# Kernel optimization log

Hardware: AMD Instinct MI355X
Metric: run time of the kernel (lower is better)

The kernel has to match this reference:

```python
import jax, jax.numpy as jnp
import numpy as np

DIM = 2048
NUM_HEADS = 16
NUM_KV_HEADS = 4
HEAD_DIM = DIM // NUM_HEADS
KV_DIM = NUM_KV_HEADS * HEAD_DIM
ROPE_BASE = 10000.0
QK_GAIN_INIT = 1.0
BSZ, SEQ = 4, 2048


def rms_norm(x):
    eps = jnp.finfo(x.dtype).eps
    return x * jax.lax.rsqrt(jnp.mean(x * x, axis=-1, keepdims=True) + eps)


def rope_cos_sin(seqlen, head_dim, base, dtype):
    inv_freq = base ** (-jnp.arange(0, head_dim, 2, dtype=jnp.float32) / head_dim)
    t = jnp.arange(seqlen, dtype=jnp.float32)
    freqs = t[:, None] * inv_freq[None, :]  # [S, hd/2]
    return jnp.cos(freqs).astype(dtype), jnp.sin(freqs).astype(dtype)


def apply_rotary(x, cos, sin):
    # x: [B, H, S, hd]; cos/sin: [S, hd/2]
    x1, x2 = jnp.split(x, 2, axis=-1)
    c = cos[None, None, :, :]
    s = sin[None, None, :, :]
    return jnp.concatenate([x1 * c + x2 * s, -x1 * s + x2 * c], axis=-1)


def setup_inputs() -> dict:
    key = jax.random.key(0)
    ks = jax.random.split(key, 6)
    std = 0.02
    return {
        "x": jax.random.normal(ks[0], (BSZ, SEQ, DIM), dtype=jnp.float32),
        "Wq": jax.random.normal(ks[1], (DIM, DIM), dtype=jnp.float32) * std,
        "Wk": jax.random.normal(ks[2], (KV_DIM, DIM), dtype=jnp.float32) * std,
        "Wv": jax.random.normal(ks[3], (KV_DIM, DIM), dtype=jnp.float32) * std,
        "Wo": jax.random.normal(ks[4], (DIM, DIM), dtype=jnp.float32) * std,
        "q_gain": jnp.full((NUM_HEADS,), QK_GAIN_INIT, dtype=jnp.float32),
    }


def reference(x, Wq, Wk, Wv, Wo, q_gain):
    bsz, seqlen, dim = x.shape
    # QKV projections (F.linear: x @ W.T)
    q = (x @ Wq.T).reshape(bsz, seqlen, NUM_HEADS, HEAD_DIM).transpose(0, 2, 1, 3)
    k = (x @ Wk.T).reshape(bsz, seqlen, NUM_KV_HEADS, HEAD_DIM).transpose(0, 2, 1, 3)
    v = (x @ Wv.T).reshape(bsz, seqlen, NUM_KV_HEADS, HEAD_DIM).transpose(0, 2, 1, 3)
    # QK RMSNorm
    q = rms_norm(q)
    k = rms_norm(k)
    # RoPE
    cos, sin = rope_cos_sin(seqlen, HEAD_DIM, ROPE_BASE, q.dtype)
    q = apply_rotary(q, cos, sin)
    k = apply_rotary(k, cos, sin)
    # per-head gain
    q = q * q_gain.astype(q.dtype)[None, :, None, None]
    # GQA: repeat kv heads
    rep = NUM_HEADS // NUM_KV_HEADS
    k = jnp.repeat(k, rep, axis=1)
    v = jnp.repeat(v, rep, axis=1)
    # causal SDPA
    scale = 1.0 / jnp.sqrt(jnp.asarray(HEAD_DIM, dtype=q.dtype))
    scores = jnp.einsum("bhsd,bhtd->bhst", q, k) * scale
    causal = jnp.tril(jnp.ones((seqlen, seqlen), dtype=bool))
    scores = jnp.where(causal[None, None], scores, jnp.asarray(-jnp.inf, scores.dtype))
    attn = jax.nn.softmax(scores, axis=-1)
    y = jnp.einsum("bhst,bhtd->bhsd", attn, v)
    y = y.transpose(0, 2, 1, 3).reshape(bsz, seqlen, dim)
    return y @ Wo.T
```

## Files before the change

kernel.cpp:

```cpp
#include <hip/hip_runtime.h>
#include <hip/hip_bf16.h>

typedef __hip_bfloat16 bf16;
typedef short s16x8 __attribute__((ext_vector_type(8)));
typedef float f32x4 __attribute__((ext_vector_type(4)));

#define DIM 2048
#define NHEADS 16
#define NKVH 4
#define HD 128
#define KVDIM 512
#define BSZ 4
#define SEQ 2048
#define MROWS (BSZ*SEQ)
#define NQKV (DIM+2*KVDIM)

__device__ __forceinline__ void gld_lds16(const bf16* g, short* l) {
  __builtin_amdgcn_global_load_lds((__attribute__((address_space(1))) void*)(void*)g,
                                   (__attribute__((address_space(3))) void*)l, 16, 0, 0);
}

__global__ __launch_bounds__(256) void cast_bf16(const float* __restrict__ src,
                                                 bf16* __restrict__ dst, int n8) {
  int i = blockIdx.x*256 + threadIdx.x;
  if (i >= n8) return;
  const float4* s4 = (const float4*)src;
  float4 a = s4[2*i];
  float4 b = s4[2*i+1];
  union { bf16 h[8]; uint4 u; } o;
  o.h[0] = __float2bfloat16(a.x); o.h[1] = __float2bfloat16(a.y);
  o.h[2] = __float2bfloat16(a.z); o.h[3] = __float2bfloat16(a.w);
  o.h[4] = __float2bfloat16(b.x); o.h[5] = __float2bfloat16(b.y);
  o.h[6] = __float2bfloat16(b.z); o.h[7] = __float2bfloat16(b.w);
  ((uint4*)dst)[i] = o.u;
}

__global__ __launch_bounds__(256) void cast_w3(const float* __restrict__ Wq,
                                               const float* __restrict__ Wk,
                                               const float* __restrict__ Wv,
                                               bf16* __restrict__ dst) {
  int i = blockIdx.x*256 + threadIdx.x;
  const float* src; int j;
  if (i < 524288)      { src = Wq; j = i; }
  else if (i < 655360) { src = Wk; j = i - 524288; }
  else                 { src = Wv; j = i - 655360; }
  const float4* s4 = (const float4*)src;
  float4 a = s4[2*j];
  float4 b = s4[2*j+1];
  union { bf16 h[8]; uint4 u; } o;
  o.h[0] = __float2bfloat16(a.x); o.h[1] = __float2bfloat16(a.y);
  o.h[2] = __float2bfloat16(a.z); o.h[3] = __float2bfloat16(a.w);
  o.h[4] = __float2bfloat16(b.x); o.h[5] = __float2bfloat16(b.y);
  o.h[6] = __float2bfloat16(b.z); o.h[7] = __float2bfloat16(b.w);
  ((uint4*)dst)[i] = o.u;
}


template<int MQ>
__device__ __forceinline__ void lda(s16x8 (&af)[4][2], const short* pa, int rds) {
#pragma unroll
  for (int fr = 0; fr < 4; fr++)
#pragma unroll
    for (int ks = 0; ks < 2; ks++)
      af[fr][ks] = *(const s16x8*)(pa + ((MQ*4 + fr)*2 + ks)*512 + rds);
}
template<int NQ>
__device__ __forceinline__ void ldb(s16x8 (&bfv)[2][2], const short* pb, int bsub, int rds) {
#pragma unroll
  for (int fc = 0; fc < 2; fc++)
#pragma unroll
    for (int ks = 0; ks < 2; ks++)
      bfv[fc][ks] = *(const s16x8*)(pb + (bsub + (NQ*2 + fc)*2 + ks)*512 + rds);
}
template<int MQ, int NQ>
__device__ __forceinline__ void mmq(f32x4 (&acc)[8][4], const s16x8 (&af)[4][2],
                                    const s16x8 (&bfv)[2][2]) {
#pragma unroll
  for (int fr = 0; fr < 4; fr++)
#pragma unroll
    for (int fc = 0; fc < 2; fc++)
#pragma unroll
      for (int ks = 0; ks < 2; ks++)
        acc[MQ*4+fr][NQ*2+fc] = __builtin_amdgcn_mfma_f32_16x16x32_bf16(
            af[fr][ks], bfv[fc][ks], acc[MQ*4+fr][NQ*2+fc], 0, 0, 0);
}

#define WV6 asm volatile("s_waitcnt vmcnt(6)" ::: "memory")
#define WV0 asm volatile("s_waitcnt vmcnt(0)" ::: "memory")
#define WVN ((void)0)
#define GBAR __builtin_amdgcn_s_barrier()
#define WLK asm volatile("s_waitcnt lgkmcnt(0)" ::: "memory")
#define PRI1 __builtin_amdgcn_s_setprio(1)
#define PRI0 __builtin_amdgcn_s_setprio(0)

#define KT(B_, T_, S1_, S2_, WVX) do {                                          \
    const short* pa = pAr[B_];                                                  \
    const short* pb = pBr[B_];                                                  \
    s16x8 af[4][2], b0f[2][2], b1f[2][2];                                       \
                                                        \
    lda<0>(af, pa, rds); ldb<0>(b0f, pb, bsub, rds);                            \
    if (S1_) {                                                                  \
      gld_lds16(Ab +      (long)((T_)+1)*64 + eA1, &L[1-(B_)][0][4096+wid512]); \
      gld_lds16(Ab + h1 + (long)((T_)+1)*64 + eA1, &L[1-(B_)][1][4096+wid512]); \
    }                                                                           \
    GBAR; WLK; PRI1; mmq<0,0>(acc, af, b0f); PRI0; GBAR;                        \
                                                        \
    ldb<1>(b1f, pb, bsub, rds);                                                 \
    if (S2_) {                                                                  \
      gld_lds16(Ab +      (long)((T_)+2)*64 + eA0, &L[B_][0][wid512]);          \
      gld_lds16(Ab + h1 + (long)((T_)+2)*64 + eA0, &L[B_][1][wid512]);          \
    }                                                                           \
    GBAR; WLK; PRI1; mmq<0,1>(acc, af, b1f); PRI0; GBAR;                        \
                                                        \
    lda<1>(af, pa, rds);                                                        \
    if (S2_) {                                                                  \
      gld_lds16(Bb + (long)((T_)+2)*64 + eA0, &L[B_][2][wid512]);               \
      gld_lds16(Bb + (long)((T_)+2)*64 + eA1, &L[B_][2][4096+wid512]);          \
    }                                                                           \
    GBAR; WLK; PRI1; mmq<1,0>(acc, af, b0f); PRI0; GBAR;                        \
                                                        \
    if (S2_) {                                                                  \
      gld_lds16(Bb + h1 + (long)((T_)+2)*64 + eA0, &L[B_][3][wid512]);          \
      gld_lds16(Bb + h1 + (long)((T_)+2)*64 + eA1, &L[B_][3][4096+wid512]);     \
    }                                                                           \
    WVX;                                                                        \
    GBAR; PRI1; mmq<1,1>(acc, af, b1f); PRI0; GBAR;                             \
  } while (0)

template<int EPI>
__global__ __launch_bounds__(512, 2) void gemm8(
    const bf16* __restrict__ A, const bf16* __restrict__ Bm,
    float* __restrict__ Cf, bf16* __restrict__ Qo, bf16* __restrict__ Ko,
    bf16* __restrict__ Vo, int N, int K) {
  __shared__ short L[2][4][8192] __attribute__((aligned(16)));
  const int tid = threadIdx.x;
  const int lane = tid & 63, wid = tid >> 6;
  const int quad = lane >> 4, l15 = lane & 15;
  const int wm = wid >> 2, wn = wid & 3;
  const int m0 = blockIdx.y * 256, n0 = blockIdx.x * 256;

  const int rds = l15*32 + ((quad*8) ^ ((l15 & 8) << 1));
  const int bsub = (wn & 1) * 8;

  const int colx = ((lane & 3) * 8) ^ ((lane >> 5) << 4);
  const int gc   = ((wid & 1) << 5) + colx;
  const int gr0  = ((wid >> 1) << 4) + (lane >> 2);
  const long eA0 = (long)gr0 * K + gc;
  const long eA1 = eA0 + 64L * K;
  const int wid512 = wid * 512;
  const bf16* Ab = A  + (long)m0 * K;
  const bf16* Bb = Bm + (long)n0 * K;
  const long h1 = 128L * K;

  const short* pAr[2] = { &L[0][wm][0], &L[1][wm][0] };
  const short* pBr[2] = { &L[0][2 + (wn >> 1)][0], &L[1][2 + (wn >> 1)][0] };

  f32x4 acc[8][4] = {};

  gld_lds16(Ab + eA0,           &L[0][0][wid512]);
  gld_lds16(Ab + eA1,           &L[0][0][4096 + wid512]);
  gld_lds16(Ab + h1 + eA0,      &L[0][1][wid512]);
  gld_lds16(Ab + h1 + eA1,      &L[0][1][4096 + wid512]);
  gld_lds16(Bb + eA0,           &L[0][2][wid512]);
  gld_lds16(Bb + eA1,           &L[0][2][4096 + wid512]);
  gld_lds16(Bb + h1 + eA0,      &L[0][3][wid512]);
  gld_lds16(Bb + h1 + eA1,      &L[0][3][4096 + wid512]);
  gld_lds16(Ab + 64 + eA0,      &L[1][0][wid512]);
  gld_lds16(Ab + h1 + 64 + eA0, &L[1][1][wid512]);
  gld_lds16(Bb + 64 + eA0,      &L[1][2][wid512]);
  gld_lds16(Bb + 64 + eA1,      &L[1][2][4096 + wid512]);
  gld_lds16(Bb + h1 + 64 + eA0, &L[1][3][wid512]);
  gld_lds16(Bb + h1 + 64 + eA1, &L[1][3][4096 + wid512]);
  WV6;
  GBAR;

  for (int t = 0; t < 30; t += 2) {
    KT(0, t,   1, 1, WV6);
    KT(1, t+1, 1, 1, WV6);
  }
  KT(0, 30, 1, 0, WV0);
  KT(1, 31, 0, 0, WVN);

#pragma unroll
  for (int mi = 0; mi < 8; mi++) {
#pragma unroll
    for (int nj = 0; nj < 4; nj++) {
      const int col = n0 + wn*64 + nj*16 + l15;
#pragma unroll
      for (int r = 0; r < 4; r++) {
        const int row = m0 + wm*128 + mi*16 + quad*4 + r;
        const float v = acc[mi][nj][r];
        if (EPI == 0) {
          Cf[(long)row*N + col] = v;
        } else {
          const int b = row >> 11, s = row & (SEQ-1);
          const bf16 hv = __float2bfloat16(v);
          if (col < DIM) {
            const int h = col >> 7, d = col & 127;
            Qo[((long)(b*NHEADS + h)*SEQ + s)*HD + d] = hv;
          } else if (col < DIM + KVDIM) {
            const int c2 = col - DIM, h = c2 >> 7, d = c2 & 127;
            Ko[((long)(b*NKVH + h)*SEQ + s)*HD + d] = hv;
          } else {
            const int c2 = col - DIM - KVDIM, h = c2 >> 7, d = c2 & 127;
            Vo[((long)(b*NKVH + h)*HD + d)*SEQ + s] = hv;
          }
        }
      }
    }
  }
}

__global__ __launch_bounds__(256) void norm_rope(bf16* __restrict__ Qb,
                                                 bf16* __restrict__ Kb,
                                                 const float* __restrict__ gain) {
  const int lane = threadIdx.x & 63, wid = threadIdx.x >> 6;
  const long rid = (long)blockIdx.x*4 + wid;
  const long QR = (long)BSZ*NHEADS*SEQ;
  bf16* ptr; float g; int s;
  if (rid < QR) {
    ptr = Qb + rid*HD;
    s = (int)(rid & (SEQ-1));
    const int h = (int)((rid >> 11) & 15);
    g = gain[h] * 0.08838834764831845f;
  } else {
    const long r2 = rid - QR;
    ptr = Kb + r2*HD;
    s = (int)(r2 & (SEQ-1));
    g = 1.0f;
  }
  float x1 = __bfloat162float(ptr[lane]);
  float x2 = __bfloat162float(ptr[lane+64]);
  float ss = x1*x1 + x2*x2;
#pragma unroll
  for (int off = 1; off < 64; off <<= 1) ss += __shfl_xor(ss, off);
  const float rn = rsqrtf(ss*(1.0f/128.0f) + 1.1920928955078125e-07f);
  const float inv_freq = exp2f((float)lane * -0.20762050593046014f);
  float sn, cs;
  sincosf((float)s * inv_freq, &sn, &cs);
  const float q1 = x1*rn, q2 = x2*rn;
  ptr[lane]    = __float2bfloat16((q1*cs + q2*sn)*g);
  ptr[lane+64] = __float2bfloat16((q2*cs - q1*sn)*g);
}

__global__ __launch_bounds__(256, 2) void attn(
    const bf16* __restrict__ Qb, const bf16* __restrict__ Kb,
    const bf16* __restrict__ Vtg, bf16* __restrict__ Yb) {
  __shared__ short Kt[64*136]  __attribute__((aligned(16)));
  __shared__ short Vt[128*72]  __attribute__((aligned(16)));
  __shared__ short Pt[4*2304]  __attribute__((aligned(16)));

  const int tid = threadIdx.x;
  const int lane = tid & 63, wid = tid >> 6;
  const int quad = lane >> 4, l15 = lane & 15;
  const int xb = blockIdx.x;
  const int bh = blockIdx.y;
  const int b = bh >> 4, h = bh & 15, kvh = h >> 2;

  const bf16* kbase = Kb  + (long)(b*NKVH + kvh)*SEQ*HD;
  const bf16* vbase = Vtg + (long)(b*NKVH + kvh)*HD*SEQ;
  short* pw0 = Pt + wid*2304;
  short* pw1 = pw0 + 1152;
  const int krow = tid >> 4, kc = (tid & 15)*8;
  const int vrow = tid >> 3, vc = (tid & 7)*8;

  for (int phase = 0; phase < 2; phase++) {
    const int qt = phase ? xb : (15 - xb);
    const int q0 = qt*128 + wid*16 + l15;
    const int q1 = q0 + 64;
    const bf16* qr0 = Qb + ((long)(b*NHEADS + h)*SEQ + q0)*HD + quad*8;
    s16x8 qa0[4], qa1[4];
#pragma unroll
    for (int st = 0; st < 4; st++) {
      qa0[st] = *(const s16x8*)(qr0 + st*32);
      qa1[st] = *(const s16x8*)(qr0 + 64*HD + st*32);
    }

    f32x4 o0[8] = {}, o1[8] = {};
    float li0 = 0.0f, li1 = 0.0f;
    const int ktiles = 2*qt + 2;

    for (int kt = 0; kt < ktiles; kt++) {
      __syncthreads();
#pragma unroll
      for (int i = 0; i < 4; i++) {
        uint4 kv = *(const uint4*)(kbase + (long)(kt*64 + i*16 + krow)*HD + kc);
        *(uint4*)&Kt[(i*16 + krow)*136 + kc] = kv;
      }
#pragma unroll
      for (int i = 0; i < 4; i++) {
        uint4 vv = *(const uint4*)(vbase + (long)(i*32 + vrow)*SEQ + kt*64 + vc);
        *(uint4*)&Vt[(i*32 + vrow)*72 + vc] = vv;
      }
      __syncthreads();

      f32x4 s0[4] = {}, s1[4] = {};
#pragma unroll
      for (int nt = 0; nt < 4; nt++) {
        s16x8 kf[4];
#pragma unroll
        for (int st = 0; st < 4; st++)
          kf[st] = *(const s16x8*)&Kt[(nt*16 + l15)*136 + st*32 + quad*8];
#pragma unroll
        for (int st = 0; st < 4; st++) {
          s0[nt] = __builtin_amdgcn_mfma_f32_16x16x32_bf16(kf[st], qa0[st], s0[nt], 0, 0, 0);
          s1[nt] = __builtin_amdgcn_mfma_f32_16x16x32_bf16(kf[st], qa1[st], s1[nt], 0, 0, 0);
        }
      }

      const bool d0 = (kt >= 2*qt);
      const bool d1 = (kt >  2*qt);
      const int tb = kt*64 + quad*4;
      union { bf16 h[16]; unsigned long long u[4]; } p0, p1;
      float rs0 = 0.0f, rs1 = 0.0f;
#pragma unroll
      for (int nt = 0; nt < 4; nt++) {
#pragma unroll
        for (int r = 0; r < 4; r++) {
          const int t = tb + nt*16 + r;
          float v0 = s0[nt][r], v1 = s1[nt][r];
          if (d0 && (t > q0)) v0 = -1e30f;
          if (d1 && (t > q1)) v1 = -1e30f;
          const float e0 = __expf(v0 - 12.0f);
          const float e1 = __expf(v1 - 12.0f);
          rs0 += e0; rs1 += e1;
          p0.h[nt*4+r] = __float2bfloat16(e0);
          p1.h[nt*4+r] = __float2bfloat16(e1);
        }
      }
      li0 += rs0; li1 += rs1;
#pragma unroll
      for (int nt = 0; nt < 4; nt++) {
        *(unsigned long long*)&pw0[l15*72 + nt*16 + quad*4] = p0.u[nt];
        *(unsigned long long*)&pw1[l15*72 + nt*16 + quad*4] = p1.u[nt];
      }

#pragma unroll
      for (int st = 0; st < 2; st++) {
        s16x8 pf0 = *(const s16x8*)&pw0[l15*72 + st*32 + quad*8];
        s16x8 pf1 = *(const s16x8*)&pw1[l15*72 + st*32 + quad*8];
#pragma unroll
        for (int dt = 0; dt < 8; dt++) {
          s16x8 vf = *(const s16x8*)&Vt[(dt*16 + l15)*72 + st*32 + quad*8];
          o0[dt] = __builtin_amdgcn_mfma_f32_16x16x32_bf16(vf, pf0, o0[dt], 0, 0, 0);
          o1[dt] = __builtin_amdgcn_mfma_f32_16x16x32_bf16(vf, pf1, o1[dt], 0, 0, 0);
        }
      }
    }

    li0 += __shfl_xor(li0, 16); li0 += __shfl_xor(li0, 32);
    li1 += __shfl_xor(li1, 16); li1 += __shfl_xor(li1, 32);
    const float inv0 = 1.0f / li0, inv1 = 1.0f / li1;

    short* ep = pw0;
#pragma unroll
    for (int g = 0; g < 2; g++) {
      const float inv = g ? inv1 : inv0;
      const f32x4* o = g ? o1 : o0;
      const int qg = g ? q1 : q0;
#pragma unroll
      for (int dt = 0; dt < 8; dt++) {
        union { bf16 h[4]; unsigned long long u; } pk;
        pk.h[0] = __float2bfloat16(o[dt][0]*inv);
        pk.h[1] = __float2bfloat16(o[dt][1]*inv);
        pk.h[2] = __float2bfloat16(o[dt][2]*inv);
        pk.h[3] = __float2bfloat16(o[dt][3]*inv);
        *(unsigned long long*)&ep[l15*136 + dt*16 + quad*4] = pk.u;
      }
      bf16* yb = Yb + ((long)(b*SEQ + qg - l15))*DIM + h*HD;
#pragma unroll
      for (int p = 0; p < 4; p++) {
        const int c = quad + 4*p;
        uint4 yv = *(const uint4*)&ep[l15*136 + c*8];
        *(uint4*)&yb[(long)l15*DIM + c*8] = yv;
      }
    }
  }
}

extern "C" void kernel_launch(void* const* d_in, const int* in_sizes, int n_in,
                              void* d_out, int out_size, void* d_ws, size_t ws_size,
                              hipStream_t stream) {
  (void)in_sizes; (void)n_in; (void)out_size; (void)ws_size;
  const float* x   = (const float*)d_in[0];
  const float* Wq  = (const float*)d_in[1];
  const float* Wk  = (const float*)d_in[2];
  const float* Wv  = (const float*)d_in[3];
  const float* Wo  = (const float*)d_in[4];
  const float* qg  = (const float*)d_in[5];

  char* ws = (char*)d_ws;
  bf16* xbf  = (bf16*)(ws);
  bf16* Wqkv = (bf16*)(ws + 33554432);
  bf16* Wob  = (bf16*)(ws + 46137344);
  bf16* Qb   = (bf16*)(ws + 54525952);
  bf16* Kb   = (bf16*)(ws + 88080384);
  bf16* Vb   = (bf16*)(ws + 96468992);
  bf16* Yb   = (bf16*)(ws + 104857600);

  cast_bf16<<<8192, 256, 0, stream>>>(x,  xbf, MROWS*DIM/8);
  cast_w3<<<3072, 256, 0, stream>>>(Wq, Wk, Wv, Wqkv);
  cast_bf16<<<2048, 256, 0, stream>>>(Wo, Wob, DIM*DIM/8);

  gemm8<1><<<dim3(NQKV/256, MROWS/256), 512, 0, stream>>>(
      xbf, Wqkv, nullptr, Qb, Kb, Vb, NQKV, DIM);

  norm_rope<<<40960, 256, 0, stream>>>(Qb, Kb, qg);

  attn<<<dim3(8, BSZ*NHEADS), 256, 0, stream>>>(Qb, Kb, Vb, Yb);

  gemm8<0><<<dim3(DIM/256, MROWS/256), 512, 0, stream>>>(
      Yb, Wob, (float*)d_out, nullptr, nullptr, nullptr, DIM, DIM);
}
```

Measured before the change: 472.4 us.

## Fuse cast kernels, swizzle GEMM block order, vectorize QKV epilogue stores via LDS

Merges the three fp32-to-bf16 cast launches into one kernel. Remaps GEMM block indices so that consecutive blocks are spread across groups of eight, which is likely meant to improve L2 reuse across XCDs. Rewrites the QKV GEMM epilogue so Q and K tiles are staged through LDS and written as 16-byte rows, and V transposed stores are packed as 8-byte runs instead of scalar bf16 stores. The LDS staging reuses the pipeline buffers without a barrier, relying on each wave having its own region. The swizzle assumes the block count divides evenly by eight.

New measurement: 439.4 us. -7.0%, faster.

```diff
diff --git a/kernel.cpp b/kernel.cpp
--- a/kernel.cpp
+++ b/kernel.cpp
@@ -20,39 +20,27 @@
                                    (__attribute__((address_space(3))) void*)l, 16, 0, 0);
 }
 
-__global__ __launch_bounds__(256) void cast_bf16(const float* __restrict__ src,
-                                                 bf16* __restrict__ dst, int n8) {
-  int i = blockIdx.x*256 + threadIdx.x;
-  if (i >= n8) return;
-  const float4* s4 = (const float4*)src;
-  float4 a = s4[2*i];
-  float4 b = s4[2*i+1];
-  union { bf16 h[8]; uint4 u; } o;
-  o.h[0] = __float2bfloat16(a.x); o.h[1] = __float2bfloat16(a.y);
-  o.h[2] = __float2bfloat16(a.z); o.h[3] = __float2bfloat16(a.w);
-  o.h[4] = __float2bfloat16(b.x); o.h[5] = __float2bfloat16(b.y);
-  o.h[6] = __float2bfloat16(b.z); o.h[7] = __float2bfloat16(b.w);
-  ((uint4*)dst)[i] = o.u;
-}
-
-__global__ __launch_bounds__(256) void cast_w3(const float* __restrict__ Wq,
-                                               const float* __restrict__ Wk,
-                                               const float* __restrict__ Wv,
-                                               bf16* __restrict__ dst) {
-  int i = blockIdx.x*256 + threadIdx.x;
-  const float* src; int j;
-  if (i < 524288)      { src = Wq; j = i; }
-  else if (i < 655360) { src = Wk; j = i - 524288; }
-  else                 { src = Wv; j = i - 655360; }
+__global__ __launch_bounds__(256) void cast_all(
+    const float* __restrict__ x,  const float* __restrict__ Wq,
+    const float* __restrict__ Wk, const float* __restrict__ Wv,
+    const float* __restrict__ Wo, bf16* __restrict__ xbf,
+    bf16* __restrict__ Wqkv, bf16* __restrict__ Wob) {
+  const int i = blockIdx.x*256 + threadIdx.x;
+  const float* src; bf16* dst; int j, o;
+  if (i < 2097152)      { src = x;  dst = xbf;  j = i;           o = i; }
+  else if (i < 2621440) { src = Wq; dst = Wqkv; j = i - 2097152; o = i - 2097152; }
+  else if (i < 2752512) { src = Wk; dst = Wqkv; j = i - 2621440; o = i - 2097152; }
+  else if (i < 2883584) { src = Wv; dst = Wqkv; j = i - 2752512; o = i - 2097152; }
+  else                  { src = Wo; dst = Wob;  j = i - 2883584; o = i - 2883584; }
   const float4* s4 = (const float4*)src;
   float4 a = s4[2*j];
   float4 b = s4[2*j+1];
-  union { bf16 h[8]; uint4 u; } o;
-  o.h[0] = __float2bfloat16(a.x); o.h[1] = __float2bfloat16(a.y);
-  o.h[2] = __float2bfloat16(a.z); o.h[3] = __float2bfloat16(a.w);
-  o.h[4] = __float2bfloat16(b.x); o.h[5] = __float2bfloat16(b.y);
-  o.h[6] = __float2bfloat16(b.z); o.h[7] = __float2bfloat16(b.w);
-  ((uint4*)dst)[i] = o.u;
+  union { bf16 h[8]; uint4 u; } pk;
+  pk.h[0] = __float2bfloat16(a.x); pk.h[1] = __float2bfloat16(a.y);
+  pk.h[2] = __float2bfloat16(a.z); pk.h[3] = __float2bfloat16(a.w);
+  pk.h[4] = __float2bfloat16(b.x); pk.h[5] = __float2bfloat16(b.y);
+  pk.h[6] = __float2bfloat16(b.z); pk.h[7] = __float2bfloat16(b.w);
+  ((uint4*)dst)[o] = pk.u;
 }
 
 
@@ -137,7 +125,12 @@
   const int lane = tid & 63, wid = tid >> 6;
   const int quad = lane >> 4, l15 = lane & 15;
   const int wm = wid >> 2, wn = wid & 3;
-  const int m0 = blockIdx.y * 256, n0 = blockIdx.x * 256;
+
+  const int gx  = gridDim.x;
+  const int lin = blockIdx.y * gx + blockIdx.x;
+  const int cpx = (gx * gridDim.y) >> 3;
+  const int swz = (lin & 7) * cpx + (lin >> 3);
+  const int m0 = (swz / gx) * 256, n0 = (swz % gx) * 256;
 
   const int rds = l15*32 + ((quad*8) ^ ((l15 & 8) << 1));
   const int bsub = (wn & 1) * 8;
@@ -181,32 +174,58 @@
   KT(0, 30, 1, 0, WV0);
   KT(1, 31, 0, 0, WVN);
 
-#pragma unroll
-  for (int mi = 0; mi < 8; mi++) {
-#pragma unroll
-    for (int nj = 0; nj < 4; nj++) {
-      const int col = n0 + wn*64 + nj*16 + l15;
-#pragma unroll
-      for (int r = 0; r < 4; r++) {
-        const int row = m0 + wm*128 + mi*16 + quad*4 + r;
-        const float v = acc[mi][nj][r];
-        if (EPI == 0) {
-          Cf[(long)row*N + col] = v;
-        } else {
-          const int b = row >> 11, s = row & (SEQ-1);
-          const bf16 hv = __float2bfloat16(v);
-          if (col < DIM) {
-            const int h = col >> 7, d = col & 127;
-            Qo[((long)(b*NHEADS + h)*SEQ + s)*HD + d] = hv;
-          } else if (col < DIM + KVDIM) {
-            const int c2 = col - DIM, h = c2 >> 7, d = c2 & 127;
-            Ko[((long)(b*NKVH + h)*SEQ + s)*HD + d] = hv;
-          } else {
-            const int c2 = col - DIM - KVDIM, h = c2 >> 7, d = c2 & 127;
-            Vo[((long)(b*NKVH + h)*HD + d)*SEQ + s] = hv;
-          }
+  const int colg0 = n0 + wn*64;
+  const int bb = (m0 + wm*128) >> 11;
+  const int sb = (m0 + wm*128) & (SEQ-1);
+  if (EPI == 0) {
+#pragma unroll
+    for (int mi = 0; mi < 8; mi++)
+#pragma unroll
+      for (int nj = 0; nj < 4; nj++) {
+        const int col = colg0 + nj*16 + l15;
+#pragma unroll
+        for (int r = 0; r < 4; r++)
+          Cf[(long)(m0 + wm*128 + mi*16 + quad*4 + r)*N + col] = acc[mi][nj][r];
+      }
+  } else if (colg0 >= DIM + KVDIM) {
+    const int cv = colg0 - (DIM + KVDIM);
+    const int h  = cv >> 7;
+    const int db = cv & 127;
+    bf16* vb = Vo + ((long)(bb*NKVH + h)*HD)*SEQ + sb;
+#pragma unroll
+    for (int mi = 0; mi < 8; mi++)
+#pragma unroll
+      for (int nj = 0; nj < 4; nj++) {
+        const int d = db + nj*16 + l15;
+        union { bf16 h4[4]; unsigned long long u; } pk;
+        pk.h4[0] = __float2bfloat16(acc[mi][nj][0]);
+        pk.h4[1] = __float2bfloat16(acc[mi][nj][1]);
+        pk.h4[2] = __float2bfloat16(acc[mi][nj][2]);
+        pk.h4[3] = __float2bfloat16(acc[mi][nj][3]);
+        *(unsigned long long*)(vb + (long)d*SEQ + mi*16 + quad*4) = pk.u;
+      }
+  } else {
+    short* ew = &L[0][0][0] + wid*8192;
+#pragma unroll
+    for (int mi = 0; mi < 8; mi++)
+#pragma unroll
+      for (int nj = 0; nj < 4; nj++)
+#pragma unroll
+        for (int r = 0; r < 4; r++) {
+          bf16 hv = __float2bfloat16(acc[mi][nj][r]);
+          ew[(mi*16 + quad*4 + r)*64 + nj*16 + l15] = *(short*)&hv;
         }
-      }
+    asm volatile("" ::: "memory");
+    bf16* gb;
+    if (colg0 < DIM) gb = Qo + (long)(bb*NHEADS + (colg0 >> 7))*SEQ*HD;
+    else             gb = Ko + (long)(bb*NKVH + ((colg0 - DIM) >> 7))*SEQ*HD;
+    const int db = colg0 & 127;
+    const int rr = lane >> 3, c8 = (lane & 7)*8;
+#pragma unroll
+    for (int it = 0; it < 16; it++) {
+      const int row = it*8 + rr;
+      uint4 v = *(const uint4*)&ew[row*64 + c8];
+      *(uint4*)(gb + (long)(sb + row)*HD + db + c8) = v;
     }
   }
 }
@@ -398,9 +417,7 @@
   bf16* Vb   = (bf16*)(ws + 96468992);
   bf16* Yb   = (bf16*)(ws + 104857600);
 
-  cast_bf16<<<8192, 256, 0, stream>>>(x,  xbf, MROWS*DIM/8);
-  cast_w3<<<3072, 256, 0, stream>>>(Wq, Wk, Wv, Wqkv);
-  cast_bf16<<<2048, 256, 0, stream>>>(Wo, Wob, DIM*DIM/8);
+  cast_all<<<13312, 256, 0, stream>>>(x, Wq, Wk, Wv, Wo, xbf, Wqkv, Wob);
 
   gemm8<1><<<dim3(NQKV/256, MROWS/256), 512, 0, stream>>>(
       xbf, Wqkv, nullptr, Qb, Kb, Vb, NQKV, DIM);
```
